# Kernel optimization log

Measured on AMD Instinct MI355X. Metric: run time of the kernel, lower is better.

Reference implementation:

```python
import jax, jax.numpy as jnp
import numpy as np

B, T, D = 2, 1024, 2048
H, HKV, DH = 16, 4, 128
G = H // HKV  # GQA groups
F = 5632
ROPE_THETA = 10000.0
EPS = 1e-6


def _rope_tables(t, dh, theta):
    inv = 1.0 / (theta ** (np.arange(0, dh, 2, dtype=np.float32) / dh))  # [dh//2]
    ang = np.outer(np.arange(t, dtype=np.float32), inv)                  # [T, dh//2]
    return jnp.asarray(np.cos(ang)), jnp.asarray(np.sin(ang))


def setup_inputs() -> dict:
    key = jax.random.key(0)
    ks = jax.random.split(key, 9)
    s = 0.02
    cos, sin = _rope_tables(T, DH, ROPE_THETA)
    return {
        "x": jax.random.normal(ks[0], (B, T, D), jnp.float32),
        "freqs_cos": cos,
        "freqs_sin": sin,
        "w_norm1": jnp.ones((D,), jnp.float32),
        "w_norm2": jnp.ones((D,), jnp.float32),
        "wq": jax.random.normal(ks[1], (D, H * DH), jnp.float32) * s,
        "wk": jax.random.normal(ks[2], (D, HKV * DH), jnp.float32) * s,
        "wv": jax.random.normal(ks[3], (D, HKV * DH), jnp.float32) * s,
        "wo": jax.random.normal(ks[4], (D, D), jnp.float32) * s,
        "w1": jax.random.normal(ks[5], (D, F), jnp.float32) * s,
        "w2": jax.random.normal(ks[6], (F, D), jnp.float32) * s,
        "w3": jax.random.normal(ks[7], (D, F), jnp.float32) * s,
    }


def _rmsnorm(x, w):
    var = jnp.mean(jnp.square(x), axis=-1, keepdims=True)
    return x * jax.lax.rsqrt(var + EPS) * w


def _apply_rope(x, cos, sin):
    # x: [B, T, nH, DH]; cos/sin: [T, DH//2]
    xr = x.reshape(*x.shape[:-1], DH // 2, 2)
    x0, x1 = xr[..., 0], xr[..., 1]
    c = cos[None, :, None, :]
    s = sin[None, :, None, :]
    o0 = x0 * c - x1 * s
    o1 = x0 * s + x1 * c
    return jnp.stack([o0, o1], axis=-1).reshape(x.shape)


def reference(x, freqs_cos, freqs_sin, w_norm1, w_norm2, wq, wk, wv, wo, w1, w2, w3):
    residual = x
    xn = _rmsnorm(x, w_norm1)
    q = (xn @ wq).reshape(B, T, H, DH)
    k = (xn @ wk).reshape(B, T, HKV, DH)
    v = (xn @ wv).reshape(B, T, HKV, DH)
    q = _apply_rope(q, freqs_cos, freqs_sin)
    k = _apply_rope(k, freqs_cos, freqs_sin)
    # grouped heads: q -> [B, HKV, G, T, DH]; k,v -> [B, HKV, T, DH]
    q = q.transpose(0, 2, 1, 3).reshape(B, HKV, G, T, DH)
    k = k.transpose(0, 2, 1, 3)
    v = v.transpose(0, 2, 1, 3)
    scale = DH ** -0.5
    scores = jnp.einsum("bkgtd,bksd->bkgts", q, k) * scale  # [B,HKV,G,T,T]
    causal = jnp.tril(jnp.ones((T, T), dtype=bool))
    scores = jnp.where(causal, scores, -jnp.inf)
    attn = jax.nn.softmax(scores, axis=-1)
    out = jnp.einsum("bkgts,bksd->bkgtd", attn, v)  # [B,HKV,G,T,DH]
    out = out.reshape(B, H, T, DH).transpose(0, 2, 1, 3).reshape(B, T, D)
    x = residual + out @ wo
    h = _rmsnorm(x, w_norm2)
    ffn = (jax.nn.silu(h @ w1) * (h @ w3)) @ w2
    return x + ffn
```

## Files before the change

### kernel.cpp

```cpp
#include <hip/hip_runtime.h>
#include <hip/hip_bf16.h>
#include <math.h>

typedef __hip_bfloat16 bf16;
typedef __attribute__((ext_vector_type(8))) short bf16x8;
typedef __attribute__((ext_vector_type(4))) float f32x4;

__device__ __forceinline__ float b2f(bf16 v) { return __bfloat162float(v); }
__device__ __forceinline__ bf16  f2b(float v) { return __float2bfloat16(v); }

constexpr int Bc = 2, Tc = 1024, Dc = 2048, Hc = 16, HKVc = 4, DHc = 128, Fc = 5632;
constexpr int Mr = Bc * Tc;
constexpr int Nqkv = Hc * DHc + 2 * HKVc * DHc;

__device__ __forceinline__ void g2l16(void* lds, const void* g) {
  __builtin_amdgcn_global_load_lds(
      (const __attribute__((address_space(1))) unsigned int*)g,
      (__attribute__((address_space(3))) unsigned int*)lds, 16, 0, 0);
}

__global__ __launch_bounds__(256) void tcast_k(const float* __restrict__ src,
                                               bf16* __restrict__ dst,
                                               int N, int K) {
  __shared__ bf16 tile[64][68];
  const int t = threadIdx.x;
  const int n0 = blockIdx.x * 64, k0 = blockIdx.y * 64;
#pragma unroll
  for (int it = 0; it < 4; ++it) {
    const int kl = it * 16 + (t >> 4);
    const int nl = (t & 15) * 4;
    float4 v = *reinterpret_cast<const float4*>(src + (size_t)(k0 + kl) * N + n0 + nl);
    tile[kl][nl]     = f2b(v.x);
    tile[kl][nl + 1] = f2b(v.y);
    tile[kl][nl + 2] = f2b(v.z);
    tile[kl][nl + 3] = f2b(v.w);
  }
  __syncthreads();
  union { uint4 u; bf16 h[8]; } o;
#pragma unroll
  for (int it = 0; it < 2; ++it) {
    const int nl = it * 32 + (t >> 3);
    const int kl = (t & 7) * 8;
#pragma unroll
    for (int j = 0; j < 8; ++j) o.h[j] = tile[kl + j][nl];
    *reinterpret_cast<uint4*>(dst + (size_t)(n0 + nl) * K + k0 + kl) = o.u;
  }
}

__global__ __launch_bounds__(256) void tcast_ffn(const float* __restrict__ src,
                                                 bf16* __restrict__ dst,
                                                 int off) {
  __shared__ bf16 tile[64][68];
  const int t = threadIdx.x;
  const int n0 = blockIdx.x * 64, k0 = blockIdx.y * 64;
#pragma unroll
  for (int it = 0; it < 4; ++it) {
    const int kl = it * 16 + (t >> 4);
    const int nl = (t & 15) * 4;
    float4 v = *reinterpret_cast<const float4*>(src + (size_t)(k0 + kl) * Fc + n0 + nl);
    tile[kl][nl]     = f2b(v.x);
    tile[kl][nl + 1] = f2b(v.y);
    tile[kl][nl + 2] = f2b(v.z);
    tile[kl][nl + 3] = f2b(v.w);
  }
  __syncthreads();
  union { uint4 u; bf16 h[8]; } o;
#pragma unroll
  for (int it = 0; it < 2; ++it) {
    const int nl = it * 32 + (t >> 3);
    const int kl = (t & 7) * 8;
#pragma unroll
    for (int j = 0; j < 8; ++j) o.h[j] = tile[kl + j][nl];
    const int n = n0 + nl;
    const int r = ((n >> 4) << 5) + (n & 15) + off;
    *reinterpret_cast<uint4*>(dst + (size_t)r * Dc + k0 + kl) = o.u;
  }
}

__global__ __launch_bounds__(256) void copy_f32(const float* __restrict__ src,
                                                float* __restrict__ dst) {
  const int i = blockIdx.x * 256 + threadIdx.x;
  reinterpret_cast<float4*>(dst)[i] = reinterpret_cast<const float4*>(src)[i];
}

__global__ __launch_bounds__(256) void rmsnorm_k(const float* __restrict__ x,
                                                 const float* __restrict__ w,
                                                 bf16* __restrict__ out) {
  const size_t rbase = (size_t)blockIdx.x * Dc;
  float ss = 0.f;
  for (int i = threadIdx.x; i < Dc; i += 256) {
    float v = x[rbase + i];
    ss += v * v;
  }
#pragma unroll
  for (int off = 32; off > 0; off >>= 1) ss += __shfl_down(ss, off, 64);
  __shared__ float red[4];
  const int lane = threadIdx.x & 63, wid = threadIdx.x >> 6;
  if (lane == 0) red[wid] = ss;
  __syncthreads();
  const float scale = rsqrtf((red[0] + red[1] + red[2] + red[3]) / (float)Dc + 1e-6f);
  for (int i = threadIdx.x; i < Dc; i += 256)
    out[rbase + i] = f2b(x[rbase + i] * scale * w[i]);
}

template <bool ADDRES>
__global__ __launch_bounds__(256) void gemm128(const bf16* __restrict__ A,
                                               const bf16* __restrict__ Bt,
                                               const float* __restrict__ Res,
                                               void* __restrict__ Out,
                                               int N, int K) {
  __shared__ __align__(16) bf16 As[128 * 32];
  __shared__ __align__(16) bf16 Bs[128 * 32];
  const int t = threadIdx.x;
  const int bm = blockIdx.y * 128, bn = blockIdx.x * 128;
  const int lane = t & 63, wv = t >> 6;
  const int wm = (wv & 1) * 64, wn = (wv >> 1) * 64;
  const int sr = t >> 2, sc = (t & 3) * 8;
  const bf16* ga = A + (size_t)(bm + sr) * K + sc;
  const bf16* gb = Bt + (size_t)(bn + sr) * K + sc;
  bf16* lA0 = As + sr * 32 + sc;
  bf16* lA1 = As + (64 + sr) * 32 + sc;
  bf16* lB0 = Bs + sr * 32 + sc;
  bf16* lB1 = Bs + (64 + sr) * 32 + sc;
  const size_t rstep = (size_t)64 * K;
  f32x4 acc[4][4] = {};
  const int fr = lane & 15, fko = (lane >> 4) * 8;
  for (int k0 = 0; k0 < K; k0 += 32) {
    __syncthreads();
    g2l16(lA0, ga + k0);
    g2l16(lA1, ga + rstep + k0);
    g2l16(lB0, gb + k0);
    g2l16(lB1, gb + rstep + k0);
    __syncthreads();
    bf16x8 af[4], bff[4];
#pragma unroll
    for (int i = 0; i < 4; ++i)
      af[i] = *reinterpret_cast<const bf16x8*>(As + (wm + i * 16 + fr) * 32 + fko);
#pragma unroll
    for (int j = 0; j < 4; ++j)
      bff[j] = *reinterpret_cast<const bf16x8*>(Bs + (wn + j * 16 + fr) * 32 + fko);
#pragma unroll
    for (int i = 0; i < 4; ++i)
#pragma unroll
      for (int j = 0; j < 4; ++j)
        acc[i][j] = __builtin_amdgcn_mfma_f32_16x16x32_bf16(af[i], bff[j], acc[i][j], 0, 0, 0);
  }
  const int er = (lane >> 4) * 4, ec = lane & 15;
#pragma unroll
  for (int i = 0; i < 4; ++i)
#pragma unroll
    for (int j = 0; j < 4; ++j) {
      const int row = bm + wm + i * 16 + er;
      const int col = bn + wn + j * 16 + ec;
#pragma unroll
      for (int r = 0; r < 4; ++r) {
        const size_t idx = (size_t)(row + r) * N + col;
        if (ADDRES) ((float*)Out)[idx] = Res[idx] + acc[i][j][r];
        else        ((bf16*)Out)[idx] = f2b(acc[i][j][r]);
      }
    }
}

template <int K>
__global__ __launch_bounds__(512, 2) void ffn_gemm256(const bf16* __restrict__ A,
                                                      const bf16* __restrict__ B,
                                                      bf16* __restrict__ act) {
  constexpr int NT = K / 64;
  constexpr int NIT = NT / 2;
  __shared__ bf16 As[2 * 256 * 64];
  __shared__ bf16 Bs[3 * 256 * 64];
  const int tid = threadIdx.x;
  const int lane = tid & 63, wv = tid >> 6;
  const int wr = wv >> 2, wc = wv & 3;
  const int fr = lane & 15, quad = lane >> 4;
  const int swz = fr & 7;
  const int bm = blockIdx.y * 256;
  const int bn = blockIdx.x * 256;
  const int lrow = tid >> 3;
  const int scol = ((tid & 7) ^ (lrow & 7)) * 8;
  const size_t rstep = (size_t)64 * K;

  auto stageA = [&](int t, int half) {
    const int buf = (t & 1) * 16384;
    const bf16* g = A + (size_t)(bm + half * 128 + lrow) * K + t * 64 + scol;
    bf16* d = As + buf + half * 8192 + (size_t)tid * 8;
    g2l16(d, g);
    g2l16(d + 4096, g + rstep);
  };
  auto stageB = [&](int t, int half, int buf) {
    const bf16* g = B + (size_t)(bn + half * 128 + lrow) * K + t * 64 + scol;
    bf16* d = Bs + buf * 16384 + half * 8192 + (size_t)tid * 8;
    g2l16(d, g);
    g2l16(d + 4096, g + rstep);
  };

  f32x4 acc[8][4] = {};
  const int u0 = (quad ^ swz) * 8;

  stageA(0, 0); stageA(0, 1);
  stageB(0, 0, 0); stageB(0, 1, 0);
  stageB(1, 0, 1); stageB(1, 1, 1);
  asm volatile("s_waitcnt vmcnt(4)" ::: "memory");
  __builtin_amdgcn_s_barrier();

  int rb0 = 0, rb1 = 1, sb = 2;
  for (int it = 0; it < NIT; ++it) {
    const int t1 = 2 * it + 1;
#pragma unroll
    for (int j = 0; j < 8; ++j) {
      const int bufT = (j < 4) ? 0 : 16384;
      const int bufB = ((j < 4) ? rb0 : rb1) * 16384;
      const int qr4 = ((j & 3) >> 1) * 4, qc2 = ((j & 3) & 1) * 2;
      bf16x8 af[4][2], bv[2][2];
      const bf16* Ab = As + bufT + (size_t)(wr * 128 + fr) * 64;
      const bf16* Bb = Bs + bufB + (size_t)(wc * 64 + fr) * 64;
#pragma unroll
      for (int ii = 0; ii < 4; ++ii) {
        af[ii][0] = *reinterpret_cast<const bf16x8*>(Ab + (qr4 + ii) * 1024 + u0);
        af[ii][1] = *reinterpret_cast<const bf16x8*>(Ab + (qr4 + ii) * 1024 + (u0 ^ 32));
      }
#pragma unroll
      for (int jj = 0; jj < 2; ++jj) {
        bv[jj][0] = *reinterpret_cast<const bf16x8*>(Bb + (qc2 + jj) * 1024 + u0);
        bv[jj][1] = *reinterpret_cast<const bf16x8*>(Bb + (qc2 + jj) * 1024 + (u0 ^ 32));
      }
      if (j == 0)      stageA(t1, 0);
      else if (j == 1) stageA(t1, 1);
      else if (j == 2) { if (2 * it + 2 < NT) stageB(2 * it + 2, 0, sb); }
      else if (j == 3) { if (2 * it + 2 < NT) stageB(2 * it + 2, 1, sb); }
      else if (j == 4) { if (2 * it + 2 < NT) stageA(2 * it + 2, 0); }
      else if (j == 5) { if (2 * it + 2 < NT) stageA(2 * it + 2, 1); }
      else if (j == 6) { if (2 * it + 3 < NT) stageB(2 * it + 3, 0, rb0); }
      else             { if (2 * it + 3 < NT) stageB(2 * it + 3, 1, rb0); }
      __builtin_amdgcn_s_barrier();
      asm volatile("s_waitcnt lgkmcnt(0)" ::: "memory");
      __builtin_amdgcn_sched_barrier(0);
      __builtin_amdgcn_s_setprio(1);
#pragma unroll
      for (int ii = 0; ii < 4; ++ii)
#pragma unroll
        for (int jj = 0; jj < 2; ++jj) {
          acc[qr4 + ii][qc2 + jj] = __builtin_amdgcn_mfma_f32_16x16x32_bf16(
              af[ii][0], bv[jj][0], acc[qr4 + ii][qc2 + jj], 0, 0, 0);
          acc[qr4 + ii][qc2 + jj] = __builtin_amdgcn_mfma_f32_16x16x32_bf16(
              af[ii][1], bv[jj][1], acc[qr4 + ii][qc2 + jj], 0, 0, 0);
        }
      __builtin_amdgcn_s_setprio(0);
      if (j == 3) {
        if (2 * it + 2 < NT) asm volatile("s_waitcnt vmcnt(4)" ::: "memory");
        else                 asm volatile("s_waitcnt vmcnt(0)" ::: "memory");
      } else if (j == 7) {
        if (2 * it + 3 < NT)      asm volatile("s_waitcnt vmcnt(4)" ::: "memory");
        else if (2 * it + 2 < NT) asm volatile("s_waitcnt vmcnt(0)" ::: "memory");
      }
      __builtin_amdgcn_s_barrier();
    }
    const int nrb0 = sb; sb = rb1; rb1 = rb0; rb0 = nrb0;
  }

  const int er = quad * 4, ec = lane & 15;
#pragma unroll
  for (int i = 0; i < 8; ++i) {
    const int row = bm + wr * 128 + i * 16 + er;
#pragma unroll
    for (int jp = 0; jp < 2; ++jp) {
      const f32x4 g = acc[i][2 * jp], u = acc[i][2 * jp + 1];
      const int f = blockIdx.x * 128 + wc * 32 + jp * 16 + ec;
#pragma unroll
      for (int r = 0; r < 4; ++r) {
        const float sg = g[r] / (1.f + __expf(-g[r]));
        act[(size_t)(row + r) * Fc + f] = f2b(sg * u[r]);
      }
    }
  }
}

template <int KFULL, int KSUB>
__global__ __launch_bounds__(512, 2) void gemm256sk(const bf16* __restrict__ A,
                                                    const bf16* __restrict__ Bt,
                                                    float* __restrict__ Out,
                                                    int N) {
  constexpr int NT = KSUB / 64;
  constexpr int NIT = NT / 2;
  __shared__ bf16 As[2 * 256 * 64];
  __shared__ bf16 Bs[3 * 256 * 64];
  const int tid = threadIdx.x;
  const int lane = tid & 63, wv = tid >> 6;
  const int wr = wv >> 2, wc = wv & 3;
  const int fr = lane & 15, quad = lane >> 4;
  const int swz = fr & 7;
  const int bm = blockIdx.y * 256;
  const int bn = blockIdx.x * 256;
  const int kbase = blockIdx.z * KSUB;
  const int lrow = tid >> 3;
  const int scol = ((tid & 7) ^ (lrow & 7)) * 8;
  const size_t rstep = (size_t)64 * KFULL;

  auto stageA = [&](int t, int half) {
    const int buf = (t & 1) * 16384;
    const bf16* g = A + (size_t)(bm + half * 128 + lrow) * KFULL + kbase + t * 64 + scol;
    bf16* d = As + buf + half * 8192 + (size_t)tid * 8;
    g2l16(d, g);
    g2l16(d + 4096, g + rstep);
  };
  auto stageB = [&](int t, int half, int buf) {
    const bf16* g = Bt + (size_t)(bn + half * 128 + lrow) * KFULL + kbase + t * 64 + scol;
    bf16* d = Bs + buf * 16384 + half * 8192 + (size_t)tid * 8;
    g2l16(d, g);
    g2l16(d + 4096, g + rstep);
  };

  f32x4 acc[8][4] = {};
  const int u0 = (quad ^ swz) * 8;

  stageA(0, 0); stageA(0, 1);
  stageB(0, 0, 0); stageB(0, 1, 0);
  stageB(1, 0, 1); stageB(1, 1, 1);
  asm volatile("s_waitcnt vmcnt(4)" ::: "memory");
  __builtin_amdgcn_s_barrier();

  int rb0 = 0, rb1 = 1, sb = 2;
  for (int it = 0; it < NIT; ++it) {
    const int t1 = 2 * it + 1;
#pragma unroll
    for (int j = 0; j < 8; ++j) {
      const int bufT = (j < 4) ? 0 : 16384;
      const int bufB = ((j < 4) ? rb0 : rb1) * 16384;
      const int qr4 = ((j & 3) >> 1) * 4, qc2 = ((j & 3) & 1) * 2;
      bf16x8 af[4][2], bv[2][2];
      const bf16* Ab = As + bufT + (size_t)(wr * 128 + fr) * 64;
      const bf16* Bb = Bs + bufB + (size_t)(wc * 64 + fr) * 64;
#pragma unroll
      for (int ii = 0; ii < 4; ++ii) {
        af[ii][0] = *reinterpret_cast<const bf16x8*>(Ab + (qr4 + ii) * 1024 + u0);
        af[ii][1] = *reinterpret_cast<const bf16x8*>(Ab + (qr4 + ii) * 1024 + (u0 ^ 32));
      }
#pragma unroll
      for (int jj = 0; jj < 2; ++jj) {
        bv[jj][0] = *reinterpret_cast<const bf16x8*>(Bb + (qc2 + jj) * 1024 + u0);
        bv[jj][1] = *reinterpret_cast<const bf16x8*>(Bb + (qc2 + jj) * 1024 + (u0 ^ 32));
      }
      if (j == 0)      stageA(t1, 0);
      else if (j == 1) stageA(t1, 1);
      else if (j == 2) { if (2 * it + 2 < NT) stageB(2 * it + 2, 0, sb); }
      else if (j == 3) { if (2 * it + 2 < NT) stageB(2 * it + 2, 1, sb); }
      else if (j == 4) { if (2 * it + 2 < NT) stageA(2 * it + 2, 0); }
      else if (j == 5) { if (2 * it + 2 < NT) stageA(2 * it + 2, 1); }
      else if (j == 6) { if (2 * it + 3 < NT) stageB(2 * it + 3, 0, rb0); }
      else             { if (2 * it + 3 < NT) stageB(2 * it + 3, 1, rb0); }
      __builtin_amdgcn_s_barrier();
      asm volatile("s_waitcnt lgkmcnt(0)" ::: "memory");
      __builtin_amdgcn_sched_barrier(0);
      __builtin_amdgcn_s_setprio(1);
#pragma unroll
      for (int ii = 0; ii < 4; ++ii)
#pragma unroll
        for (int jj = 0; jj < 2; ++jj) {
          acc[qr4 + ii][qc2 + jj] = __builtin_amdgcn_mfma_f32_16x16x32_bf16(
              af[ii][0], bv[jj][0], acc[qr4 + ii][qc2 + jj], 0, 0, 0);
          acc[qr4 + ii][qc2 + jj] = __builtin_amdgcn_mfma_f32_16x16x32_bf16(
              af[ii][1], bv[jj][1], acc[qr4 + ii][qc2 + jj], 0, 0, 0);
        }
      __builtin_amdgcn_s_setprio(0);
      if (j == 3) {
        if (2 * it + 2 < NT) asm volatile("s_waitcnt vmcnt(4)" ::: "memory");
        else                 asm volatile("s_waitcnt vmcnt(0)" ::: "memory");
      } else if (j == 7) {
        if (2 * it + 3 < NT)      asm volatile("s_waitcnt vmcnt(4)" ::: "memory");
        else if (2 * it + 2 < NT) asm volatile("s_waitcnt vmcnt(0)" ::: "memory");
      }
      __builtin_amdgcn_s_barrier();
    }
    const int nrb0 = sb; sb = rb1; rb1 = rb0; rb0 = nrb0;
  }

  const int er = quad * 4, ec = lane & 15;
#pragma unroll
  for (int i = 0; i < 8; ++i) {
    const int row = bm + wr * 128 + i * 16 + er;
#pragma unroll
    for (int jc = 0; jc < 4; ++jc) {
      const int col = bn + wc * 64 + jc * 16 + ec;
#pragma unroll
      for (int r = 0; r < 4; ++r)
        atomicAdd(&Out[(size_t)(row + r) * N + col], acc[i][jc][r]);
    }
  }
}

__global__ __launch_bounds__(256) void repack_k(const bf16* __restrict__ qkv,
                                                const float* __restrict__ cosb,
                                                const float* __restrict__ sinb,
                                                bf16* __restrict__ Qr,
                                                bf16* __restrict__ Kr,
                                                bf16* __restrict__ Vt) {
  const int bt = blockIdx.x;
  const int b = bt >> 10, tp = bt & (Tc - 1);
  const int t0 = threadIdx.x;
  const bf16* row = qkv + (size_t)bt * Nqkv;
#pragma unroll
  for (int k = 0; k < 4; ++k) {
    int p2 = k * 256 + t0;
    int hh = p2 >> 6, i = p2 & 63;
    float c = cosb[tp * 64 + i], sn = sinb[tp * 64 + i];
    float x0 = b2f(row[hh * 128 + 2 * i]), x1 = b2f(row[hh * 128 + 2 * i + 1]);
    bf16* dst = Qr + ((size_t)(b * Hc + hh) * Tc + tp) * DHc + 2 * i;
    dst[0] = f2b(x0 * c - x1 * sn);
    dst[1] = f2b(x0 * sn + x1 * c);
  }
  {
    int hh = t0 >> 6, i = t0 & 63;
    float c = cosb[tp * 64 + i], sn = sinb[tp * 64 + i];
    float x0 = b2f(row[2048 + hh * 128 + 2 * i]), x1 = b2f(row[2048 + hh * 128 + 2 * i + 1]);
    bf16* dst = Kr + ((size_t)(b * HKVc + hh) * Tc + tp) * DHc + 2 * i;
    dst[0] = f2b(x0 * c - x1 * sn);
    dst[1] = f2b(x0 * sn + x1 * c);
  }
#pragma unroll
  for (int k = 0; k < 2; ++k) {
    int e = k * 256 + t0;
    int kvh = e >> 7, dd = e & 127;
    Vt[((size_t)(b * HKVc + kvh) * DHc + dd) * Tc + tp] = row[2560 + e];
  }
}

__global__ __launch_bounds__(256) void fattn(const bf16* __restrict__ Qr,
                                             const bf16* __restrict__ Kr,
                                             const bf16* __restrict__ Vt,
                                             bf16* __restrict__ ao) {
  __shared__ __align__(16) bf16 Ks[64 * 136];
  __shared__ __align__(16) bf16 Vts[128 * 72];
  __shared__ __align__(16) bf16 Ps[4][16 * 72];
  const int idx = blockIdx.x;
  const int r = idx & 15;
  const int qt = (r & 1) ? (15 - (r >> 1)) : (r >> 1);
  const int h = (idx >> 4) & 15;
  const int b = idx >> 8;
  const int kv = h >> 2;
  const int t = threadIdx.x, lane = t & 63, wv = t >> 6;
  const int fr = lane & 15, quad = lane >> 4;

  const bf16* Qbase = Qr + ((size_t)(b * Hc + h) * Tc + qt * 64) * DHc;
  const bf16* Kbase = Kr + (size_t)(b * HKVc + kv) * Tc * DHc;
  const bf16* Vbase = Vt + (size_t)(b * HKVc + kv) * DHc * Tc;

  bf16x8 qf[4];
#pragma unroll
  for (int c = 0; c < 4; ++c)
    qf[c] = *reinterpret_cast<const bf16x8*>(Qbase + (size_t)(wv * 16 + fr) * DHc + c * 32 + quad * 8);

  float m[4], l[4];
  f32x4 o[8] = {};
#pragma unroll
  for (int r2 = 0; r2 < 4; ++r2) { m[r2] = -3.0e38f; l[r2] = 0.f; }

  for (int kt = 0; kt <= qt; ++kt) {
    __syncthreads();
    {
      const bf16* src = Kbase + (size_t)kt * 64 * DHc;
#pragma unroll
      for (int i2 = 0; i2 < 4; ++i2) {
        int flat = i2 * 256 + t;
        int row = flat >> 4, c16 = flat & 15;
        uint4 v = *reinterpret_cast<const uint4*>(src + (size_t)row * DHc + c16 * 8);
        *reinterpret_cast<uint4*>(&Ks[row * 136 + c16 * 8]) = v;
      }
#pragma unroll
      for (int i2 = 0; i2 < 4; ++i2) {
        int flat = i2 * 256 + t;
        int row = flat >> 3, c8 = flat & 7;
        uint4 v = *reinterpret_cast<const uint4*>(Vbase + (size_t)row * Tc + kt * 64 + c8 * 8);
        *reinterpret_cast<uint4*>(&Vts[row * 72 + c8 * 8]) = v;
      }
    }
    __syncthreads();
    f32x4 s[4];
#pragma unroll
    for (int cb = 0; cb < 4; ++cb) {
      f32x4 acc = {};
#pragma unroll
      for (int kc = 0; kc < 4; ++kc) {
        bf16x8 kf = *reinterpret_cast<const bf16x8*>(&Ks[(cb * 16 + fr) * 136 + kc * 32 + quad * 8]);
        acc = __builtin_amdgcn_mfma_f32_16x16x32_bf16(qf[kc], kf, acc, 0, 0, 0);
      }
      s[cb] = acc * 0.08838834764831845f;
    }
    if (kt == qt) {
#pragma unroll
      for (int cb = 0; cb < 4; ++cb)
#pragma unroll
        for (int r2 = 0; r2 < 4; ++r2) {
          int key = cb * 16 + fr;
          int qg = wv * 16 + quad * 4 + r2;
          if (key > qg) s[cb][r2] = -3.0e38f;
        }
    }
    float tm[4], ts[4];
#pragma unroll
    for (int r2 = 0; r2 < 4; ++r2)
      tm[r2] = fmaxf(fmaxf(s[0][r2], s[1][r2]), fmaxf(s[2][r2], s[3][r2]));
#pragma unroll
    for (int off = 1; off < 16; off <<= 1)
#pragma unroll
      for (int r2 = 0; r2 < 4; ++r2)
        tm[r2] = fmaxf(tm[r2], __shfl_xor(tm[r2], off, 64));
    float al[4];
#pragma unroll
    for (int r2 = 0; r2 < 4; ++r2) {
      float mn = fmaxf(m[r2], tm[r2]);
      al[r2] = __expf(m[r2] - mn);
      m[r2] = mn;
      ts[r2] = 0.f;
    }
#pragma unroll
    for (int cb = 0; cb < 4; ++cb)
#pragma unroll
      for (int r2 = 0; r2 < 4; ++r2) {
        float e = __expf(s[cb][r2] - m[r2]);
        s[cb][r2] = e;
        ts[r2] += e;
      }
#pragma unroll
    for (int off = 1; off < 16; off <<= 1)
#pragma unroll
      for (int r2 = 0; r2 < 4; ++r2)
        ts[r2] += __shfl_xor(ts[r2], off, 64);
#pragma unroll
    for (int r2 = 0; r2 < 4; ++r2) l[r2] = l[r2] * al[r2] + ts[r2];
#pragma unroll
    for (int db = 0; db < 8; ++db)
#pragma unroll
      for (int r2 = 0; r2 < 4; ++r2) o[db][r2] *= al[r2];
    bf16* pw = Ps[wv];
#pragma unroll
    for (int cb = 0; cb < 4; ++cb)
#pragma unroll
      for (int r2 = 0; r2 < 4; ++r2)
        pw[(quad * 4 + r2) * 72 + cb * 16 + fr] = f2b(s[cb][r2]);
    bf16x8 pa[2];
    pa[0] = *reinterpret_cast<const bf16x8*>(&pw[fr * 72 + quad * 8]);
    pa[1] = *reinterpret_cast<const bf16x8*>(&pw[fr * 72 + 32 + quad * 8]);
#pragma unroll
    for (int db = 0; db < 8; ++db) {
      bf16x8 v0 = *reinterpret_cast<const bf16x8*>(&Vts[(db * 16 + fr) * 72 + quad * 8]);
      bf16x8 v1 = *reinterpret_cast<const bf16x8*>(&Vts[(db * 16 + fr) * 72 + 32 + quad * 8]);
      o[db] = __builtin_amdgcn_mfma_f32_16x16x32_bf16(pa[0], v0, o[db], 0, 0, 0);
      o[db] = __builtin_amdgcn_mfma_f32_16x16x32_bf16(pa[1], v1, o[db], 0, 0, 0);
    }
  }
#pragma unroll
  for (int r2 = 0; r2 < 4; ++r2) {
    float inv = 1.f / l[r2];
    int qg = qt * 64 + wv * 16 + quad * 4 + r2;
    bf16* orow = ao + (size_t)(b * Tc + qg) * Dc + h * DHc;
#pragma unroll
    for (int db = 0; db < 8; ++db)
      orow[db * 16 + fr] = f2b(o[db][r2] * inv);
  }
}

extern "C" void kernel_launch(void* const* d_in, const int* in_sizes, int n_in,
                              void* d_out, int out_size, void* d_ws, size_t ws_size,
                              hipStream_t stream) {
  const float* x    = (const float*)d_in[0];
  const float* fcos = (const float*)d_in[1];
  const float* fsin = (const float*)d_in[2];
  const float* wn1  = (const float*)d_in[3];
  const float* wn2  = (const float*)d_in[4];
  const float* wq   = (const float*)d_in[5];
  const float* wk   = (const float*)d_in[6];
  const float* wv   = (const float*)d_in[7];
  const float* wo   = (const float*)d_in[8];
  const float* w1   = (const float*)d_in[9];
  const float* w2   = (const float*)d_in[10];
  const float* w3   = (const float*)d_in[11];

  char* p = (char*)d_ws;
  bf16* wqkv_t = (bf16*)p;                 p += (size_t)Nqkv * Dc * 2;
  bf16* qkv    = (bf16*)p;                 p += (size_t)Mr * Nqkv * 2;
  float* xat   = (float*)d_ws;
  bf16* wo_t = (bf16*)p;                   p += (size_t)Dc * Dc * 2;
  bf16* w13t = (bf16*)p;                   p += (size_t)2 * Fc * Dc * 2;
  bf16* w2t  = w13t;
  bf16* xn   = (bf16*)p;                   p += (size_t)Mr * Dc * 2;
  bf16* ao   = (bf16*)p;                   p += (size_t)Mr * Dc * 2;
  bf16* act  = (bf16*)p;                   p += (size_t)Mr * Fc * 2;
  bf16* hb = xn;
  bf16* Qr = act;
  bf16* Kr = act + (size_t)Mr * Hc * DHc;
  bf16* Vtb = Kr + (size_t)Mr * HKVc * DHc;

  const dim3 blk(256);
  tcast_k<<<dim3(32, 32), blk, 0, stream>>>(wq, wqkv_t, 2048, 2048);
  tcast_k<<<dim3(8, 32), blk, 0, stream>>>(wk, wqkv_t + (size_t)2048 * 2048, 512, 2048);
  tcast_k<<<dim3(8, 32), blk, 0, stream>>>(wv, wqkv_t + (size_t)2560 * 2048, 512, 2048);
  tcast_k<<<dim3(32, 32), blk, 0, stream>>>(wo, wo_t, 2048, 2048);
  tcast_ffn<<<dim3(88, 32), blk, 0, stream>>>(w1, w13t, 0);
  tcast_ffn<<<dim3(88, 32), blk, 0, stream>>>(w3, w13t, 16);

  rmsnorm_k<<<Mr, blk, 0, stream>>>(x, wn1, xn);
  gemm128<false><<<dim3(Nqkv / 128, Mr / 128), blk, 0, stream>>>(xn, wqkv_t, nullptr, qkv, Nqkv, Dc);
  repack_k<<<Mr, blk, 0, stream>>>(qkv, fcos, fsin, Qr, Kr, Vtb);
  fattn<<<Bc * Hc * 16, blk, 0, stream>>>(Qr, Kr, Vtb, ao);
  copy_f32<<<Mr * Dc / 1024, blk, 0, stream>>>(x, xat);
  gemm256sk<Dc, 512><<<dim3(Dc / 256, Mr / 256, 4), dim3(512), 0, stream>>>(ao, wo_t, xat, Dc);
  rmsnorm_k<<<Mr, blk, 0, stream>>>(xat, wn2, hb);
  ffn_gemm256<Dc><<<dim3(2 * Fc / 256, Mr / 256), dim3(512), 0, stream>>>(hb, w13t, act);
  tcast_k<<<dim3(32, 88), blk, 0, stream>>>(w2, w2t, 2048, 5632);
  copy_f32<<<Mr * Dc / 1024, blk, 0, stream>>>(xat, (float*)d_out);
  gemm256sk<Fc, 1408><<<dim3(Dc / 256, Mr / 256, 4), dim3(512), 0, stream>>>(act, w2t, (float*)d_out, Dc);
}
```

Measured before the change: 653.2 us.

## Replace split-K atomic accumulation with partial buffers and fused reduce kernels

The split-K GEMMs now write each K-slice's partial result to its own fp32 buffer with plain stores instead of doing atomicAdd into the output. New reduce kernels sum the four partials with the residual. For the attention-output projection the reduction is fused with the second RMSNorm, so the separate copy and rmsnorm launches go away. This removes atomic contention and two kernel launches, at the cost of a 64 MB partial buffer and extra fp32 read/write traffic for the reduction.

```diff
diff --git a/kernel.cpp b/kernel.cpp
--- a/kernel.cpp
+++ b/kernel.cpp
@@ -77,12 +77,6 @@
   }
 }
 
-__global__ __launch_bounds__(256) void copy_f32(const float* __restrict__ src,
-                                                float* __restrict__ dst) {
-  const int i = blockIdx.x * 256 + threadIdx.x;
-  reinterpret_cast<float4*>(dst)[i] = reinterpret_cast<const float4*>(src)[i];
-}
-
 __global__ __launch_bounds__(256) void rmsnorm_k(const float* __restrict__ x,
                                                  const float* __restrict__ w,
                                                  bf16* __restrict__ out) {
@@ -101,6 +95,61 @@
   const float scale = rsqrtf((red[0] + red[1] + red[2] + red[3]) / (float)Dc + 1e-6f);
   for (int i = threadIdx.x; i < Dc; i += 256)
     out[rbase + i] = f2b(x[rbase + i] * scale * w[i]);
+}
+
+__global__ __launch_bounds__(256) void reduce4_rms(const float* __restrict__ P,
+                                                   const float* __restrict__ x,
+                                                   const float* __restrict__ w,
+                                                   float* __restrict__ xat,
+                                                   bf16* __restrict__ hb) {
+  constexpr size_t PS = (size_t)Mr * Dc;
+  const size_t base4 = (size_t)blockIdx.x * (Dc / 4);
+  const int t = threadIdx.x;
+  float4 v[2];
+  float ss = 0.f;
+#pragma unroll
+  for (int j = 0; j < 2; ++j) {
+    const size_t c4 = base4 + t + j * 256;
+    float4 a = reinterpret_cast<const float4*>(x)[c4];
+#pragma unroll
+    for (int z = 0; z < 4; ++z) {
+      float4 q = reinterpret_cast<const float4*>(P + z * PS)[c4];
+      a.x += q.x; a.y += q.y; a.z += q.z; a.w += q.w;
+    }
+    reinterpret_cast<float4*>(xat)[c4] = a;
+    ss += a.x * a.x + a.y * a.y + a.z * a.z + a.w * a.w;
+    v[j] = a;
+  }
+#pragma unroll
+  for (int off = 32; off > 0; off >>= 1) ss += __shfl_down(ss, off, 64);
+  __shared__ float red[4];
+  const int lane = t & 63, wid = t >> 6;
+  if (lane == 0) red[wid] = ss;
+  __syncthreads();
+  const float scale = rsqrtf((red[0] + red[1] + red[2] + red[3]) / (float)Dc + 1e-6f);
+  bf16* hrow = hb + (size_t)blockIdx.x * Dc;
+#pragma unroll
+  for (int j = 0; j < 2; ++j) {
+    const int c = (t + j * 256) * 4;
+    hrow[c]     = f2b(v[j].x * scale * w[c]);
+    hrow[c + 1] = f2b(v[j].y * scale * w[c + 1]);
+    hrow[c + 2] = f2b(v[j].z * scale * w[c + 2]);
+    hrow[c + 3] = f2b(v[j].w * scale * w[c + 3]);
+  }
+}
+
+__global__ __launch_bounds__(256) void reduce4_add(const float* __restrict__ P,
+                                                   const float* __restrict__ res,
+                                                   float* __restrict__ out) {
+  constexpr size_t PS = (size_t)Mr * Dc;
+  const size_t c4 = (size_t)blockIdx.x * 256 + threadIdx.x;
+  float4 a = reinterpret_cast<const float4*>(res)[c4];
+#pragma unroll
+  for (int z = 0; z < 4; ++z) {
+    float4 q = reinterpret_cast<const float4*>(P + z * PS)[c4];
+    a.x += q.x; a.y += q.y; a.z += q.z; a.w += q.w;
+  }
+  reinterpret_cast<float4*>(out)[c4] = a;
 }
 
 template <bool ADDRES>
@@ -278,7 +327,7 @@
 template <int KFULL, int KSUB>
 __global__ __launch_bounds__(512, 2) void gemm256sk(const bf16* __restrict__ A,
                                                     const bf16* __restrict__ Bt,
-                                                    float* __restrict__ Out,
+                                                    float* __restrict__ Part,
                                                     int N) {
   constexpr int NT = KSUB / 64;
   constexpr int NIT = NT / 2;
@@ -374,6 +423,7 @@
     const int nrb0 = sb; sb = rb1; rb1 = rb0; rb0 = nrb0;
   }
 
+  float* P = Part + (size_t)blockIdx.z * ((size_t)Mr * N);
   const int er = quad * 4, ec = lane & 15;
 #pragma unroll
   for (int i = 0; i < 8; ++i) {
@@ -383,7 +433,7 @@
       const int col = bn + wc * 64 + jc * 16 + ec;
 #pragma unroll
       for (int r = 0; r < 4; ++r)
-        atomicAdd(&Out[(size_t)(row + r) * N + col], acc[i][jc][r]);
+        P[(size_t)(row + r) * N + col] = acc[i][jc][r];
     }
   }
 }
@@ -585,6 +635,7 @@
   bf16* xn   = (bf16*)p;                   p += (size_t)Mr * Dc * 2;
   bf16* ao   = (bf16*)p;                   p += (size_t)Mr * Dc * 2;
   bf16* act  = (bf16*)p;                   p += (size_t)Mr * Fc * 2;
+  float* Pbuf = (float*)p;                 p += (size_t)4 * Mr * Dc * 4;
   bf16* hb = xn;
   bf16* Qr = act;
   bf16* Kr = act + (size_t)Mr * Hc * DHc;
@@ -602,11 +653,10 @@
   gemm128<false><<<dim3(Nqkv / 128, Mr / 128), blk, 0, stream>>>(xn, wqkv_t, nullptr, qkv, Nqkv, Dc);
   repack_k<<<Mr, blk, 0, stream>>>(qkv, fcos, fsin, Qr, Kr, Vtb);
   fattn<<<Bc * Hc * 16, blk, 0, stream>>>(Qr, Kr, Vtb, ao);
-  copy_f32<<<Mr * Dc / 1024, blk, 0, stream>>>(x, xat);
-  gemm256sk<Dc, 512><<<dim3(Dc / 256, Mr / 256, 4), dim3(512), 0, stream>>>(ao, wo_t, xat, Dc);
-  rmsnorm_k<<<Mr, blk, 0, stream>>>(xat, wn2, hb);
+  gemm256sk<Dc, 512><<<dim3(Dc / 256, Mr / 256, 4), dim3(512), 0, stream>>>(ao, wo_t, Pbuf, Dc);
+  reduce4_rms<<<Mr, blk, 0, stream>>>(Pbuf, x, wn2, xat, hb);
   ffn_gemm256<Dc><<<dim3(2 * Fc / 256, Mr / 256), dim3(512), 0, stream>>>(hb, w13t, act);
   tcast_k<<<dim3(32, 88), blk, 0, stream>>>(w2, w2t, 2048, 5632);
-  copy_f32<<<Mr * Dc / 1024, blk, 0, stream>>>(xat, (float*)d_out);
-  gemm256sk<Fc, 1408><<<dim3(Dc / 256, Mr / 256, 4), dim3(512), 0, stream>>>(act, w2t, (float*)d_out, Dc);
-}
+  gemm256sk<Fc, 1408><<<dim3(Dc / 256, Mr / 256, 4), dim3(512), 0, stream>>>(act, w2t, Pbuf, Dc);
+  reduce4_add<<<Mr * Dc / 1024, blk, 0, stream>>>(Pbuf, xat, (float*)d_out);
+}
```

After: 571.8 us. 12.5% less time.
